# Kernel optimization log

Hardware: AMD Instinct MI355X
Metric: run time of the kernel (lower is better)

Reference implementation:

```python
import jax, jax.numpy as jnp
import numpy as np

LENGTH = 128
BATCH = 256
MARGIN = 1.0
BONUS = 1000.0  # constraint bump applied to chart cells
NCELLS = LENGTH * (LENGTH + 1) // 2
NCONSTR = 8


def _offsets(length):
    off = np.zeros(length, dtype=np.int64)
    for lvl in range(1, length):
        off[lvl] = off[lvl - 1] + (length - (lvl - 1))
    return off

OFF = _offsets(LENGTH)


def _level_child_indices(length):
    # For each level: flat chart indices of left/right children, shape (L, N)
    idx = {}
    for level in range(1, length):
        L = length - level
        pos = np.arange(L)[:, None]
        n = np.arange(level)[None, :]
        l_idx = OFF[n] + pos                      # left child span (pos, width n)
        r_idx = OFF[level - 1 - n] + pos + n + 1  # right child span
        idx[level] = (jnp.asarray(l_idx), jnp.asarray(r_idx))
    return idx

IDX = _level_child_indices(LENGTH)


def _score_offsets(length):
    soff, acc = {}, 0
    for level in range(1, length):
        soff[level] = acc
        acc += (length - level) * level
    return soff, acc

SOFF, TOTAL = _score_offsets(LENGTH)


def setup_inputs():
    key = jax.random.key(0)
    k1, k2 = jax.random.split(key)
    scores = jax.random.normal(k1, (BATCH, TOTAL), dtype=jnp.float32)
    # constrained spans at level >= 1 (original skips level <= 0)
    constraint_pos = jax.random.randint(k2, (BATCH, NCONSTR), LENGTH, NCELLS, dtype=jnp.int32)
    return {"scores": scores, "constraint_pos": constraint_pos}


def _cky(scores, chart):
    # max-plus semiring inside DP, level by level over the triangular chart
    B = chart.shape[0]
    for level in range(1, LENGTH):
        L = LENGTH - level
        N = level
        l_idx, r_idx = IDX[level]
        ls = chart[:, l_idx]                                     # (B, L, N)
        rs = chart[:, r_idx]                                     # (B, L, N)
        xs = scores[:, SOFF[level]:SOFF[level] + L * N].reshape(B, L, N)
        best = jnp.max(ls + rs + xs, axis=2)                     # (B, L)
        off = int(OFF[level])
        chart = chart.at[:, off:off + L].add(best)
    return chart[:, -1]                                          # (B,) root scores


def reference(scores, constraint_pos):
    B = scores.shape[0]
    zero_chart = jnp.zeros((B, NCELLS), dtype=scores.dtype)
    rows = jnp.arange(B)[:, None]
    constr_chart = zero_chart.at[rows, constraint_pos].set(BONUS)
    subtract = jnp.full((B,), BONUS * constraint_pos.shape[1], dtype=scores.dtype)
    constr_s = _cky(scores, constr_chart) - subtract
    pred_s = _cky(scores, zero_chart)
    mask = (jnp.abs(pred_s - constr_s) >= 0.001).astype(scores.dtype)
    hinge = jnp.maximum(MARGIN + pred_s - constr_s, 0.0) * mask
    msum = mask.sum()
    return jnp.where(msum > 0.1, hinge.sum() / jnp.maximum(msum, 1.0), hinge.sum())
```

## Files before the change

### kernel.cpp

```cpp
#include <hip/hip_runtime.h>
#include <hip/hip_bf16.h>
#include <math.h>

#define LEN 128
#define NCELLS 8256
#define TOTAL 349504
#define NCONSTR 8
#define BONUS 1000.0f
#define NT 512
#define TB_TOTAL 15912
#define TB_SOFF 333592
#define TB_VEC 3978

__device__ __forceinline__ void level_barrier() {
    __builtin_amdgcn_sched_barrier(0);
    asm volatile("s_waitcnt lgkmcnt(0)\n\ts_barrier" ::: "memory");
    __builtin_amdgcn_sched_barrier(0);
}

__device__ __forceinline__ float dpp_xor1_max(float v) {
    int r = __builtin_amdgcn_update_dpp(0, __float_as_int(v), 0xB1, 0xF, 0xF, true);
    return fmaxf(v, __int_as_float(r));
}
__device__ __forceinline__ float dpp_xor2_max(float v) {
    int r = __builtin_amdgcn_update_dpp(0, __float_as_int(v), 0x4E, 0xF, 0xF, true);
    return fmaxf(v, __int_as_float(r));
}

template<int LG>
__device__ __forceinline__ void redmax2(float& a, float& b) {
    #pragma unroll
    for (int mm = (1 << LG) >> 1; mm >= 4; mm >>= 1) {
        a = fmaxf(a, __shfl_xor(a, mm));
        b = fmaxf(b, __shfl_xor(b, mm));
    }
    if constexpr (LG >= 2) { a = dpp_xor2_max(a); b = dpp_xor2_max(b); }
    if constexpr (LG >= 1) { a = dpp_xor1_max(a); b = dpp_xor1_max(b); }
}

template<int LG, int LG2, int JM, int JM2>
__device__ __forceinline__ void lstep(const int level, int& soff,
        const float* __restrict__ g, float2* __restrict__ chart,
        float (&rcur)[16], float (&rnxt)[16], const int tid)
{
    const int N = level;
    const int L = LEN - level;
    constexpr int T = 1 << LG;
    const int pos = tid >> LG;
    const int sub = tid & (T - 1);
    const int soff_n = soff + L * N;

    if constexpr (LG2 >= 0) {
        constexpr int T2 = 1 << LG2;
        const int N2 = level + 2;
        const int L2 = L - 2;
        const int soff_nn = soff_n + (L - 1) * (N + 1);
        const int pos2 = tid >> LG2;
        const int sub2 = tid & (T2 - 1);
        if (pos2 < L2) {
            const float* __restrict__ gp = g + soff_nn + pos2 * N2 + sub2;
            #pragma unroll
            for (int j = 0; j < JM2; j++) {
                if (sub2 + j * T2 < N2) rnxt[j] = gp[j * T2];
            }
        }
    }

    float bp = -INFINITY, bc = -INFINITY;
    if (pos < L) {
        const int jml = (N - sub + T - 1) >> LG;
        float2 lv[JM], rv[JM];
        float  xs[JM];
        #pragma unroll
        for (int j = 0; j < JM; j++) {
            const int n = sub + j * T;
            const int m = level - 1 - n;
            const bool v = (j < jml);
            const int l_idx = ((n * (257 - n)) >> 1) + pos;
            int r_idx = ((m * (257 - m)) >> 1) + pos + n + 1;
            r_idx = v ? r_idx : 0;
            lv[j] = chart[l_idx];
            rv[j] = chart[r_idx];
            xs[j] = v ? rcur[j] : -INFINITY;
        }
        #pragma unroll
        for (int j = 0; j < JM; j++) {
            bp = fmaxf(bp, lv[j].x + rv[j].x + xs[j]);
            bc = fmaxf(bc, lv[j].y + rv[j].y + xs[j]);
        }
    }
    redmax2<LG>(bp, bc);
    if (pos < L && sub == 0) {
        const int q = ((level * (257 - level)) >> 1) + pos;
        float2 c = chart[q];
        c.x += bp;
        c.y += bc;
        chart[q] = c;
    }
    level_barrier();
    soff = soff_n;
}

template<int K>
__device__ __forceinline__ void seg4(int& soff, const float* __restrict__ g,
        float2* __restrict__ chart, float (&X)[16], float (&Y)[16], float (&Z)[16],
        const int tid)
{
    lstep<2,2,K,K>  (4*K-3, soff, g, chart, X, Z, tid);
    lstep<2,2,K,K>  (4*K-2, soff, g, chart, Y, X, tid);
    lstep<2,2,K,K+1>(4*K-1, soff, g, chart, Z, Y, tid);
    lstep<2,2,K,K+1>(4*K,   soff, g, chart, X, Z, tid);
}

template<int LGT>
__device__ __forceinline__ void tail_level(const int level, int& tb,
        float2* __restrict__ chart, const float* __restrict__ sc, const int lane)
{
    const int N = level, L = LEN - level;
    constexpr int T = 1 << LGT;
    const int pos = lane >> LGT;
    const int sub = lane & (T - 1);
    const bool act = (pos < L);
    const int jmax = (N + T - 1) >> LGT;
    const int base = tb + pos * N;
    float bp = -INFINITY, bc = -INFINITY;
    #pragma unroll 4
    for (int j = 0; j < jmax; j++) {
        const int n = sub + j * T;
        const bool v = act && (n < N);
        const int m = level - 1 - n;
        int l_idx = ((n * (257 - n)) >> 1) + pos;
        int r_idx = ((m * (257 - m)) >> 1) + pos + n + 1;
        l_idx = v ? l_idx : 0;
        r_idx = v ? r_idx : 0;
        const float2 lv = chart[l_idx];
        const float2 rv = chart[r_idx];
        const float x = v ? sc[base + (n < N ? n : 0)] : -INFINITY;
        bp = fmaxf(bp, lv.x + rv.x + x);
        bc = fmaxf(bc, lv.y + rv.y + x);
    }
    redmax2<LGT>(bp, bc);
    if (act && sub == 0) {
        const int q = ((level * (257 - level)) >> 1) + pos;
        float2 c = chart[q];
        c.x += bp;
        c.y += bc;
        chart[q] = c;
    }
    asm volatile("s_waitcnt lgkmcnt(0)" ::: "memory");
    tb += L * N;
}

__global__ __launch_bounds__(NT)
void cky_fused_kernel(const float* __restrict__ scores,
                      const int* __restrict__ cpos,
                      float* __restrict__ ws)
{
    __shared__ float2 chart[NCELLS];
    __shared__ float4 sc4[TB_VEC];

    const int b   = blockIdx.x;
    const int tid = threadIdx.x;
    const float* __restrict__ g = scores + (size_t)b * TOTAL;

    float rA[16], rB[16], rC[16];

    float4 tt[8];
    {
        const float4* __restrict__ g4 = (const float4*)(g + TB_SOFF);
        #pragma unroll
        for (int k = 0; k < 8; k++) {
            const int i4 = tid + (k << 9);
            if (i4 < TB_VEC) tt[k] = g4[i4];
        }
    }
    {
        const int pos = tid >> 2;
        const int sub = tid & 3;
        if (pos < 127 && sub == 0) rA[0] = g[pos];
        if (pos < 126 && sub < 2)  rB[0] = g[127 + pos * 2 + sub];
    }
    int cp = 0;
    if (tid < NCONSTR) cp = cpos[b * NCONSTR + tid];

    for (int i = tid; i < NCELLS; i += NT) chart[i] = make_float2(0.f, 0.f);
    #pragma unroll
    for (int k = 0; k < 8; k++) {
        const int i4 = tid + (k << 9);
        if (i4 < TB_VEC) sc4[i4] = tt[k];
    }
    level_barrier();
    if (tid < NCONSTR) chart[cp].y = BONUS;
    level_barrier();

    int soff = 0;

    seg4<1>(soff, g, chart, rA, rB, rC, tid);
    seg4<2>(soff, g, chart, rB, rC, rA, tid);
    seg4<3>(soff, g, chart, rC, rA, rB, tid);
    seg4<4>(soff, g, chart, rA, rB, rC, tid);
    seg4<5>(soff, g, chart, rB, rC, rA, tid);
    seg4<6>(soff, g, chart, rC, rA, rB, tid);
    seg4<7>(soff, g, chart, rA, rB, rC, tid);
    seg4<8>(soff, g, chart, rB, rC, rA, tid);
    seg4<9>(soff, g, chart, rC, rA, rB, tid);
    seg4<10>(soff, g, chart, rA, rB, rC, tid);
    seg4<11>(soff, g, chart, rB, rC, rA, tid);
    seg4<12>(soff, g, chart, rC, rA, rB, tid);
    seg4<13>(soff, g, chart, rA, rB, rC, tid);
    seg4<14>(soff, g, chart, rB, rC, rA, tid);
    seg4<15>(soff, g, chart, rC, rA, rB, tid);
    lstep<2,2,16,16>(61, soff, g, chart, rA, rC, tid);
    lstep<2,3,16,8> (62, soff, g, chart, rB, rA, tid);
    lstep<2,3,16,9> (63, soff, g, chart, rC, rB, tid);
    lstep<3,3,8,9>  (64, soff, g, chart, rA, rC, tid);
    lstep<3,3,9,9>  (65, soff, g, chart, rB, rA, tid);
    lstep<3,3,9,9>  (66, soff, g, chart, rC, rB, tid);
    lstep<3,3,9,9>  (67, soff, g, chart, rA, rC, tid);
    lstep<3,3,9,9>  (68, soff, g, chart, rB, rA, tid);
    lstep<3,3,9,9>  (69, soff, g, chart, rC, rB, tid);
    lstep<3,3,9,9>  (70, soff, g, chart, rA, rC, tid);
    lstep<3,3,9,10> (71, soff, g, chart, rB, rA, tid);
    lstep<3,3,9,10> (72, soff, g, chart, rC, rB, tid);
    lstep<3,3,10,10>(73, soff, g, chart, rA, rC, tid);
    lstep<3,3,10,10>(74, soff, g, chart, rB, rA, tid);
    lstep<3,3,10,10>(75, soff, g, chart, rC, rB, tid);
    lstep<3,3,10,10>(76, soff, g, chart, rA, rC, tid);
    lstep<3,3,10,10>(77, soff, g, chart, rB, rA, tid);
    lstep<3,3,10,10>(78, soff, g, chart, rC, rB, tid);
    lstep<3,3,10,11>(79, soff, g, chart, rA, rC, tid);
    lstep<3,3,10,11>(80, soff, g, chart, rB, rA, tid);
    lstep<3,3,11,11>(81, soff, g, chart, rC, rB, tid);
    lstep<3,3,11,11>(82, soff, g, chart, rA, rC, tid);
    lstep<3,3,11,11>(83, soff, g, chart, rB, rA, tid);
    lstep<3,3,11,11>(84, soff, g, chart, rC, rB, tid);
    lstep<3,3,11,11>(85, soff, g, chart, rA, rC, tid);
    lstep<3,3,11,11>(86, soff, g, chart, rB, rA, tid);
    lstep<3,3,11,12>(87, soff, g, chart, rC, rB, tid);
    lstep<3,3,11,12>(88, soff, g, chart, rA, rC, tid);
    lstep<3,3,12,12>(89, soff, g, chart, rB, rA, tid);
    lstep<3,3,12,12>(90, soff, g, chart, rC, rB, tid);
    lstep<3,3,12,12>(91, soff, g, chart, rA, rC, tid);
    lstep<3,3,12,12>(92, soff, g, chart, rB, rA, tid);
    lstep<3,3,12,12>(93, soff, g, chart, rC, rB, tid);
    lstep<3,4,12,6> (94, soff, g, chart, rA, rC, tid);
    lstep<3,4,12,7> (95, soff, g, chart, rB, rA, tid);
    lstep<4,4,6,7>  (96, soff, g, chart, rC, rB, tid);
    lstep<4,4,7,7>  (97, soff, g, chart, rA, rC, tid);
    lstep<4,4,7,7>  (98, soff, g, chart, rB, rA, tid);
    lstep<4,4,7,7>  (99, soff, g, chart, rC, rB, tid);
    lstep<4,4,7,7> (100, soff, g, chart, rA, rC, tid);
    lstep<4,4,7,7> (101, soff, g, chart, rB, rA, tid);
    lstep<4,4,7,7> (102, soff, g, chart, rC, rB, tid);
    lstep<4,4,7,7> (103, soff, g, chart, rA, rC, tid);
    lstep<4,4,7,7> (104, soff, g, chart, rB, rA, tid);
    lstep<4,4,7,7> (105, soff, g, chart, rC, rB, tid);
    lstep<4,4,7,7> (106, soff, g, chart, rA, rC, tid);
    lstep<4,4,7,7> (107, soff, g, chart, rB, rA, tid);
    lstep<4,4,7,7> (108, soff, g, chart, rC, rB, tid);
    lstep<4,4,7,7> (109, soff, g, chart, rA, rC, tid);
    lstep<4,-1,7,0>(110, soff, g, chart, rB, rA, tid);
    lstep<4,-1,7,0>(111, soff, g, chart, rC, rB, tid);

    if (tid >= 64) return;
    {
        const float* __restrict__ sc = (const float*)sc4;
        int tb = 0;
        #pragma unroll 1
        for (int l = 112; l < 120; ++l) tail_level<2>(l, tb, chart, sc, tid);
        #pragma unroll 1
        for (int l = 120; l < 124; ++l) tail_level<3>(l, tb, chart, sc, tid);
        tail_level<4>(124, tb, chart, sc, tid);
        tail_level<4>(125, tb, chart, sc, tid);
        tail_level<5>(126, tb, chart, sc, tid);
        tail_level<6>(127, tb, chart, sc, tid);
    }

    if (tid == 0) {
        const float2 f = chart[NCELLS - 1];
        const float pred   = f.x;
        const float constr = f.y - BONUS * NCONSTR;
        const float diff   = pred - constr;
        const float mask   = (fabsf(diff) >= 0.001f) ? 1.f : 0.f;
        const float hinge  = fmaxf(1.0f + diff, 0.f) * mask;
        atomicAdd(ws + 0, hinge);
        atomicAdd(ws + 1, mask);
    }
}

__global__ void final_kernel(const float* __restrict__ ws, float* __restrict__ out) {
    const float h = ws[0];
    const float m = ws[1];
    out[0] = (m > 0.1f) ? (h / fmaxf(m, 1.f)) : h;
}

extern "C" void kernel_launch(void* const* d_in, const int* in_sizes, int n_in,
                              void* d_out, int out_size, void* d_ws, size_t ws_size,
                              hipStream_t stream) {
    const float* scores = (const float*)d_in[0];
    const int*   cpos   = (const int*)d_in[1];
    float* out = (float*)d_out;
    float* ws  = (float*)d_ws;

    hipMemsetAsync(ws, 0, 2 * sizeof(float), stream);
    cky_fused_kernel<<<dim3(256), dim3(NT), 0, stream>>>(scores, cpos, ws);
    final_kernel<<<dim3(1), dim3(1), 0, stream>>>(ws, out);
}
```

Before: 169.8 us.

## Run final CKY levels with all 512 threads instead of single-wave tail

Removes the single-wavefront tail path for levels 112-127, which preloaded tail scores into shared memory and ran with 64 lanes. Those levels now go through the generic block-wide lstep pipeline with wider per-position thread groups and register prefetch of scores. This spreads the tail reductions across 512 threads and drops the LDS staging of tail scores. In exchange it adds a block barrier per level on the last 16 levels and more reduction steps.

```diff
diff --git a/kernel.cpp b/kernel.cpp
--- a/kernel.cpp
+++ b/kernel.cpp
@@ -8,9 +8,6 @@
 #define NCONSTR 8
 #define BONUS 1000.0f
 #define NT 512
-#define TB_TOTAL 15912
-#define TB_SOFF 333592
-#define TB_VEC 3978
 
 __device__ __forceinline__ void level_barrier() {
     __builtin_amdgcn_sched_barrier(0);
@@ -112,52 +109,12 @@
     lstep<2,2,K,K+1>(4*K,   soff, g, chart, X, Z, tid);
 }
 
-template<int LGT>
-__device__ __forceinline__ void tail_level(const int level, int& tb,
-        float2* __restrict__ chart, const float* __restrict__ sc, const int lane)
-{
-    const int N = level, L = LEN - level;
-    constexpr int T = 1 << LGT;
-    const int pos = lane >> LGT;
-    const int sub = lane & (T - 1);
-    const bool act = (pos < L);
-    const int jmax = (N + T - 1) >> LGT;
-    const int base = tb + pos * N;
-    float bp = -INFINITY, bc = -INFINITY;
-    #pragma unroll 4
-    for (int j = 0; j < jmax; j++) {
-        const int n = sub + j * T;
-        const bool v = act && (n < N);
-        const int m = level - 1 - n;
-        int l_idx = ((n * (257 - n)) >> 1) + pos;
-        int r_idx = ((m * (257 - m)) >> 1) + pos + n + 1;
-        l_idx = v ? l_idx : 0;
-        r_idx = v ? r_idx : 0;
-        const float2 lv = chart[l_idx];
-        const float2 rv = chart[r_idx];
-        const float x = v ? sc[base + (n < N ? n : 0)] : -INFINITY;
-        bp = fmaxf(bp, lv.x + rv.x + x);
-        bc = fmaxf(bc, lv.y + rv.y + x);
-    }
-    redmax2<LGT>(bp, bc);
-    if (act && sub == 0) {
-        const int q = ((level * (257 - level)) >> 1) + pos;
-        float2 c = chart[q];
-        c.x += bp;
-        c.y += bc;
-        chart[q] = c;
-    }
-    asm volatile("s_waitcnt lgkmcnt(0)" ::: "memory");
-    tb += L * N;
-}
-
 __global__ __launch_bounds__(NT)
 void cky_fused_kernel(const float* __restrict__ scores,
                       const int* __restrict__ cpos,
                       float* __restrict__ ws)
 {
     __shared__ float2 chart[NCELLS];
-    __shared__ float4 sc4[TB_VEC];
 
     const int b   = blockIdx.x;
     const int tid = threadIdx.x;
@@ -165,15 +122,6 @@
 
     float rA[16], rB[16], rC[16];
 
-    float4 tt[8];
-    {
-        const float4* __restrict__ g4 = (const float4*)(g + TB_SOFF);
-        #pragma unroll
-        for (int k = 0; k < 8; k++) {
-            const int i4 = tid + (k << 9);
-            if (i4 < TB_VEC) tt[k] = g4[i4];
-        }
-    }
     {
         const int pos = tid >> 2;
         const int sub = tid & 3;
@@ -184,11 +132,6 @@
     if (tid < NCONSTR) cp = cpos[b * NCONSTR + tid];
 
     for (int i = tid; i < NCELLS; i += NT) chart[i] = make_float2(0.f, 0.f);
-    #pragma unroll
-    for (int k = 0; k < 8; k++) {
-        const int i4 = tid + (k << 9);
-        if (i4 < TB_VEC) sc4[i4] = tt[k];
-    }
     level_barrier();
     if (tid < NCONSTR) chart[cp].y = BONUS;
     level_barrier();
@@ -259,22 +202,24 @@
     lstep<4,4,7,7> (107, soff, g, chart, rB, rA, tid);
     lstep<4,4,7,7> (108, soff, g, chart, rC, rB, tid);
     lstep<4,4,7,7> (109, soff, g, chart, rA, rC, tid);
-    lstep<4,-1,7,0>(110, soff, g, chart, rB, rA, tid);
-    lstep<4,-1,7,0>(111, soff, g, chart, rC, rB, tid);
-
-    if (tid >= 64) return;
-    {
-        const float* __restrict__ sc = (const float*)sc4;
-        int tb = 0;
-        #pragma unroll 1
-        for (int l = 112; l < 120; ++l) tail_level<2>(l, tb, chart, sc, tid);
-        #pragma unroll 1
-        for (int l = 120; l < 124; ++l) tail_level<3>(l, tb, chart, sc, tid);
-        tail_level<4>(124, tb, chart, sc, tid);
-        tail_level<4>(125, tb, chart, sc, tid);
-        tail_level<5>(126, tb, chart, sc, tid);
-        tail_level<6>(127, tb, chart, sc, tid);
-    }
+    lstep<4,5,7,4> (110, soff, g, chart, rB, rA, tid);
+    lstep<4,5,7,4> (111, soff, g, chart, rC, rB, tid);
+    lstep<5,5,4,4>(112, soff, g, chart, rA, rC, tid);
+    lstep<5,5,4,4>(113, soff, g, chart, rB, rA, tid);
+    lstep<5,5,4,4>(114, soff, g, chart, rC, rB, tid);
+    lstep<5,5,4,4>(115, soff, g, chart, rA, rC, tid);
+    lstep<5,5,4,4>(116, soff, g, chart, rB, rA, tid);
+    lstep<5,5,4,4>(117, soff, g, chart, rC, rB, tid);
+    lstep<5,6,4,2>(118, soff, g, chart, rA, rC, tid);
+    lstep<5,6,4,2>(119, soff, g, chart, rB, rA, tid);
+    lstep<6,6,2,2>(120, soff, g, chart, rC, rB, tid);
+    lstep<6,6,2,2>(121, soff, g, chart, rA, rC, tid);
+    lstep<6,6,2,2>(122, soff, g, chart, rB, rA, tid);
+    lstep<6,6,2,2>(123, soff, g, chart, rC, rB, tid);
+    lstep<6,6,2,2>(124, soff, g, chart, rA, rC, tid);
+    lstep<6,6,2,2>(125, soff, g, chart, rB, rA, tid);
+    lstep<6,-1,2,0>(126, soff, g, chart, rC, rB, tid);
+    lstep<6,-1,2,0>(127, soff, g, chart, rA, rB, tid);
 
     if (tid == 0) {
         const float2 f = chart[NCELLS - 1];
```

New measurement: 143.8 us. 1.18x faster.
